# Optimization experiments

Hardware: AMD Instinct MI355X
Metric: run time of the kernel (lower is better)

Reference implementation:

```python
import jax, jax.numpy as jnp
from jax import lax
import numpy as np

B, Cin, Cout, H, W, K = 8, 128, 128, 64, 64, 3
K2 = K * K
STRIDE, PAD, DIL = 1, 1, 1
EPS = 1e-5


def setup_inputs() -> dict:
    key = jax.random.key(0)
    ks = jax.random.split(key, 9)
    fan_off = Cin * K2
    fan_def = Cin * K2
    x = jax.random.normal(ks[0], (B, Cin, H, W), jnp.float32)
    # small offset weights -> offsets of O(1) pixel, like early training
    offset_w = jax.random.normal(ks[1], (2 * K2, Cin, K, K), jnp.float32) / np.sqrt(fan_off)
    offset_b = 0.01 * jax.random.normal(ks[2], (2 * K2,), jnp.float32)
    deform_w = jax.random.normal(ks[3], (Cout, Cin, K, K), jnp.float32) / np.sqrt(fan_def)
    deform_b = 0.01 * jax.random.normal(ks[4], (Cout,), jnp.float32)
    gamma = 1.0 + 0.1 * jax.random.normal(ks[5], (Cout,), jnp.float32)
    beta = 0.1 * jax.random.normal(ks[6], (Cout,), jnp.float32)
    running_mean = 0.1 * jax.random.normal(ks[7], (Cout,), jnp.float32)
    running_var = jax.random.uniform(ks[8], (Cout,), jnp.float32, 0.5, 1.5)
    return {"x": x, "offset_w": offset_w, "offset_b": offset_b,
            "deform_w": deform_w, "deform_b": deform_b,
            "gamma": gamma, "beta": beta,
            "running_mean": running_mean, "running_var": running_var}


def _deform_block(x, offset_w, offset_b, deform_w, deform_b, gamma, beta, mean, var):
    # 1) offset prediction: standard 3x3 conv -> [B, 2*K2, Ho, Wo]
    offset = lax.conv_general_dilated(
        x, offset_w, window_strides=(STRIDE, STRIDE),
        padding=((PAD, PAD), (PAD, PAD)), rhs_dilation=(DIL, DIL),
        dimension_numbers=("NCHW", "OIHW", "NCHW"))
    offset = offset + offset_b[None, :, None, None]
    Ho, Wo = offset.shape[2], offset.shape[3]

    # torchvision layout: channel 2k -> dy, 2k+1 -> dx for kernel tap k
    off = offset.reshape(B, K2, 2, Ho, Wo)
    dy, dx = off[:, :, 0], off[:, :, 1]              # [B, K2, Ho, Wo]

    ky = (jnp.arange(K2) // K).astype(jnp.float32)
    kx = (jnp.arange(K2) % K).astype(jnp.float32)
    base_y = (jnp.arange(Ho, dtype=jnp.float32) * STRIDE - PAD)[None, :] + (ky * DIL)[:, None]  # [K2, Ho]
    base_x = (jnp.arange(Wo, dtype=jnp.float32) * STRIDE - PAD)[None, :] + (kx * DIL)[:, None]  # [K2, Wo]
    py = base_y[None, :, :, None] + dy               # [B, K2, Ho, Wo]
    px = base_x[None, :, None, :] + dx

    # 2) bilinear sampling with zero padding outside the image
    y0 = jnp.floor(py)
    x0 = jnp.floor(px)
    wy1 = py - y0; wy0 = 1.0 - wy1
    wx1 = px - x0; wx0 = 1.0 - wx1
    y0i = y0.astype(jnp.int32)
    x0i = x0.astype(jnp.int32)
    xf = x.reshape(B, Cin, H * W)

    def corner(yi, xi, wgt):
        valid = (yi >= 0) & (yi < H) & (xi >= 0) & (xi < W)
        idx = (jnp.clip(yi, 0, H - 1) * W + jnp.clip(xi, 0, W - 1)).reshape(B, 1, -1)
        g = jnp.take_along_axis(xf, idx, axis=2).reshape(B, Cin, K2, Ho, Wo)
        return g * (wgt * valid)[:, None]

    samp = (corner(y0i, x0i, wy0 * wx0)
            + corner(y0i, x0i + 1, wy0 * wx1)
            + corner(y0i + 1, x0i, wy1 * wx0)
            + corner(y0i + 1, x0i + 1, wy1 * wx1))   # [B, Cin, K2, Ho, Wo]

    # 3) conv-like accumulation over (Cin, K2)
    out = jnp.einsum("bckhw,ock->bohw", samp, deform_w.reshape(Cout, Cin, K2))
    out = out + deform_b[None, :, None, None]

    # 4) BatchNorm (inference, running stats) + SiLU
    scale = gamma / jnp.sqrt(var + EPS)
    out = (out - mean[None, :, None, None]) * scale[None, :, None, None] + beta[None, :, None, None]
    return out * jax.nn.sigmoid(out)


def reference(x, offset_w, offset_b, deform_w, deform_b, gamma, beta, running_mean, running_var):
    return _deform_block(x, offset_w, offset_b, deform_w, deform_b,
                         gamma, beta, running_mean, running_var)
```

## Files before the change

### kernel.cpp

```cpp
#include <hip/hip_runtime.h>

typedef float f32x4 __attribute__((ext_vector_type(4)));
typedef __bf16 bf16x8 __attribute__((ext_vector_type(8)));
typedef unsigned short u16x8 __attribute__((ext_vector_type(8)));

static constexpr int B_ = 8, Cin = 128, Cout = 128, K2 = 9;
static constexpr int HW  = 64 * 64;
static constexpr int CHW = Cin * HW;
static constexpr int KC  = Cin * K2;
static constexpr int SLD = 136;

static __device__ __forceinline__ unsigned short f2bf(float f) {
  unsigned int u = __builtin_bit_cast(unsigned int, f);
  u = u + 0x7fffu + ((u >> 16) & 1u);
  return (unsigned short)(u >> 16);
}
static __device__ __forceinline__ float b2f_lo(unsigned int u) {
  return __builtin_bit_cast(float, u << 16);
}
static __device__ __forceinline__ float b2f_hi(unsigned int u) {
  return __builtin_bit_cast(float, u & 0xffff0000u);
}
static __device__ __forceinline__ unsigned cvt_pk_bf16(float lo, float hi) {
  unsigned r;
  asm("v_cvt_pk_bf16_f32 %0, %1, %2" : "=v"(r) : "v"(lo), "v"(hi));
  return r;
}

__global__ __launch_bounds__(256) void prep_trans_kernel(
    const float* __restrict__ x, const float* __restrict__ dw,
    const float* __restrict__ ow, unsigned short* __restrict__ wsW2,
    unsigned short* __restrict__ wOffB2, unsigned short* __restrict__ xt) {
  int bid = blockIdx.x;
  int t = threadIdx.x;

  int swz = (bid & 7) * 64 + (bid >> 3);
  int b = swz >> 6, y = swz & 63;
  int lane = t & 63, cq = t >> 6;
  __shared__ unsigned short L[64 * SLD];
  const float* xb = x + b * CHW + y * 64;
#pragma unroll
  for (int i = 0; i < 32; ++i) {
    int c = i * 4 + cq;
    L[lane * SLD + c] = f2bf(xb[c * HW + lane]);
  }
  __syncthreads();
  int p = t >> 2, q = t & 3;
  unsigned short* op = xt + (size_t)b * HW * 128 + y * 64 * 128 + p * 128 + q * 32;
#pragma unroll
  for (int s = 0; s < 4; ++s)
    *(u16x8*)(op + s * 8) = *(const u16x8*)&L[p * SLD + q * 32 + s * 8];

  for (int i = bid * 256 + t; i < 8 * 9 * 4 * 512; i += 512 * 256) {
    int j = i & 7, ln = (i >> 3) & 63, ks = (i >> 9) & 3, t2 = i >> 11;
    int k = t2 % 9, w = t2 / 9;
    int oc = w * 16 + (ln & 15);
    int c = ks * 32 + (ln >> 4) * 8 + j;
    wsW2[i] = f2bf(dw[(oc * Cin + c) * K2 + k]);
  }
  {
    int i = bid * 256 + t;
    if (i < 9 * 4 * 2 * 512) {
      int j = i & 7, ln = (i >> 3) & 63, m = (i >> 9) & 1, t3 = i >> 10;
      int ks = t3 & 3, r = t3 >> 2;
      int oc = m * 16 + (ln & 15);
      int c = ks * 32 + (ln >> 4) * 8 + j;
      wOffB2[i] = (oc < 18) ? f2bf(ow[(oc * Cin + c) * K2 + r]) : (unsigned short)0;
    }
  }
}

__global__ __launch_bounds__(512, 4) void fused_kernel(
    const unsigned short* __restrict__ xt, const unsigned short* __restrict__ wsW2,
    const unsigned short* __restrict__ wOffB2, const float* __restrict__ ob,
    const float* __restrict__ dbias, const float* __restrict__ gamma,
    const float* __restrict__ beta, const float* __restrict__ mean,
    const float* __restrict__ var, float* __restrict__ out) {
  int bid = blockIdx.x;
  int swz = (bid & 7) * 64 + (bid >> 3);
  int b = swz >> 6, ho = swz & 63;
  int t = threadIdx.x;
  int lane = t & 63, wv = t >> 6;
  int col = lane & 15, g = lane >> 4;

  __shared__ unsigned short SAB[2][64 * SLD];
  __shared__ float T[64 * 20];
  __shared__ float RW4[576 * 4];
  __shared__ unsigned RI[576];

  const unsigned short* xtb = xt + (size_t)b * HW * 128;
  const unsigned int* xtb32 = (const unsigned int*)xtb;

  auto stageA = [&](int r, int buf) {
    int ky = r / 3, kx = r % 3;
    int yv = ho + ky - 1;
    bool oky = (unsigned)yv < 64u;
    int yc = min(max(yv, 0), 63);
#pragma unroll
    for (int rr = 0; rr < 8; ++rr) {
      int p = wv * 8 + rr;
      int xc = p + kx - 1;
      bool ok = oky && ((unsigned)xc < 64u);
      int xcc = min(max(xc, 0), 63);
      unsigned v = ok ? xtb32[(yc * 64 + xcc) * 64 + lane] : 0u;
      *(unsigned*)&SAB[buf][p * SLD + 2 * lane] = v;
    }
  };

  f32x4 accO = (f32x4){0.f, 0.f, 0.f, 0.f};
  int mA = wv >> 2, nA = wv & 3;

  stageA(0, 0);
  __syncthreads();
  for (int r = 0; r < 9; ++r) {
    int cur = r & 1;
    if (r < 8) stageA(r + 1, cur ^ 1);
#pragma unroll
    for (int ks = 0; ks < 4; ++ks) {
      bf16x8 bfr = *(const bf16x8*)&SAB[cur][(nA * 16 + col) * SLD + ks * 32 + g * 8];
      u16x8 af = *(const u16x8*)(wOffB2 + ((r * 4 + ks) * 2 + mA) * 512 + lane * 8);
      accO = __builtin_amdgcn_mfma_f32_16x16x32_bf16(
          __builtin_bit_cast(bf16x8, af), bfr, accO, 0, 0, 0);
    }
    __syncthreads();
  }
  {
#pragma unroll
    for (int rg = 0; rg < 4; ++rg) {
      int row = mA * 16 + g * 4 + rg;
      if (row < 18) T[(nA * 16 + col) * 20 + row] = accO[rg] + ob[row];
    }
  }
  __syncthreads();

#pragma unroll
  for (int it = 0; it < 2; ++it) {
    int idx = it * 64 + lane;
    if (idx < 72) {
      int k = idx >> 3, rr = idx & 7;
      int pp = wv * 8 + rr;
      float dy = T[pp * 20 + 2 * k], dx = T[pp * 20 + 2 * k + 1];
      float py = (float)(ho - 1 + k / 3) + dy;
      float px = (float)(pp - 1 + k % 3) + dx;
      float y0f = floorf(py), x0f = floorf(px);
      float wy1 = py - y0f, wy0 = 1.f - wy1;
      float wx1 = px - x0f, wx0 = 1.f - wx1;
      int y0 = (int)y0f, x0 = (int)x0f;
      bool vy0 = (unsigned)y0 < 64u, vy1 = (unsigned)(y0 + 1) < 64u;
      bool vx0 = (unsigned)x0 < 64u, vx1 = (unsigned)(x0 + 1) < 64u;
      float w00 = (vy0 && vx0) ? wy0 * wx0 : 0.f;
      float w01 = (vy0 && vx1) ? wy0 * wx1 : 0.f;
      float w10 = (vy1 && vx0) ? wy1 * wx0 : 0.f;
      float w11 = (vy1 && vx1) ? wy1 * wx1 : 0.f;
      int y0c = min(max(y0, 0), 63), y1c = min(max(y0 + 1, 0), 63);
      int xb2 = min(max(x0, 0), 62);
      unsigned pkw = (unsigned)(y0c * 64 + xb2) | ((unsigned)(y1c * 64 + xb2) << 12);
      if (x0 == 63) pkw |= (1u << 24);
      if (x0 == -1) pkw |= (1u << 25);
      int ridx = k * 64 + pp;
      RW4[ridx * 4 + 0] = w00; RW4[ridx * 4 + 1] = w01;
      RW4[ridx * 4 + 2] = w10; RW4[ridx * 4 + 3] = w11;
      RI[ridx] = pkw;
    }
  }
  __syncthreads();

  f32x4 acc[4];
#pragma unroll
  for (int j = 0; j < 4; ++j) acc[j] = (f32x4){0.f, 0.f, 0.f, 0.f};
  const unsigned short* wA = wsW2 + wv * (9 * 4 * 512) + lane * 8;

  {
#pragma unroll
    for (int r = 0; r < 8; ++r) {
      int pp = wv * 8 + r, ridx = pp;
      unsigned pk = RI[ridx];
      int o0 = pk & 4095, o1 = (pk >> 12) & 4095;
      bool s0 = (pk >> 24) & 1, s1 = (pk >> 25) & 1;
      const unsigned int* r0 = xtb32 + o0 * 64;
      const unsigned int* r1 = xtb32 + o1 * 64;
      unsigned c00 = r0[lane], c01 = r0[lane + 64];
      unsigned c10 = r1[lane], c11 = r1[lane + 64];
      unsigned a0 = s0 ? c01 : c00, a1 = s1 ? c00 : c01;
      unsigned a2 = s0 ? c11 : c10, a3 = s1 ? c10 : c11;
      float4 wv4 = *(const float4*)&RW4[ridx * 4];
      float lo = wv4.x * b2f_lo(a0) + wv4.y * b2f_lo(a1) + wv4.z * b2f_lo(a2) + wv4.w * b2f_lo(a3);
      float hi = wv4.x * b2f_hi(a0) + wv4.y * b2f_hi(a1) + wv4.z * b2f_hi(a2) + wv4.w * b2f_hi(a3);
      *(unsigned*)&SAB[0][pp * SLD + 2 * lane] = cvt_pk_bf16(lo, hi);
    }
  }
  __syncthreads();

  for (int k = 0; k < 9; ++k) {
    int cur = k & 1;
    unsigned c00[8], c01[8], c10[8], c11[8];
    if (k < 8) {
#pragma unroll
      for (int r = 0; r < 8; ++r) {
        int ridx = (k + 1) * 64 + wv * 8 + r;
        unsigned pk = RI[ridx];
        int o0 = pk & 4095, o1 = (pk >> 12) & 4095;
        const unsigned int* r0 = xtb32 + o0 * 64;
        const unsigned int* r1 = xtb32 + o1 * 64;
        c00[r] = r0[lane]; c01[r] = r0[lane + 64];
        c10[r] = r1[lane]; c11[r] = r1[lane + 64];
      }
    }
    u16x8 af[4];
#pragma unroll
    for (int ks = 0; ks < 4; ++ks)
      af[ks] = *(const u16x8*)(wA + (k * 4 + ks) * 512);
#pragma unroll
    for (int pt = 0; pt < 4; ++pt)
#pragma unroll
      for (int ks = 0; ks < 4; ++ks) {
        bf16x8 bfr = *(const bf16x8*)&SAB[cur][(pt * 16 + col) * SLD + ks * 32 + g * 8];
        acc[pt] = __builtin_amdgcn_mfma_f32_16x16x32_bf16(
            __builtin_bit_cast(bf16x8, af[ks]), bfr, acc[pt], 0, 0, 0);
      }
    if (k < 8) {
#pragma unroll
      for (int r = 0; r < 8; ++r) {
        int ridx = (k + 1) * 64 + wv * 8 + r;
        unsigned pk = RI[ridx];
        bool s0 = (pk >> 24) & 1, s1 = (pk >> 25) & 1;
        float4 wv4 = *(const float4*)&RW4[ridx * 4];
        unsigned a0 = s0 ? c01[r] : c00[r], a1 = s1 ? c00[r] : c01[r];
        unsigned a2 = s0 ? c11[r] : c10[r], a3 = s1 ? c10[r] : c11[r];
        float lo = wv4.x * b2f_lo(a0) + wv4.y * b2f_lo(a1) + wv4.z * b2f_lo(a2) + wv4.w * b2f_lo(a3);
        float hi = wv4.x * b2f_hi(a0) + wv4.y * b2f_hi(a1) + wv4.z * b2f_hi(a2) + wv4.w * b2f_hi(a3);
        *(unsigned*)&SAB[cur ^ 1][(wv * 8 + r) * SLD + 2 * lane] = cvt_pk_bf16(lo, hi);
      }
    }
    __syncthreads();
  }

  float* op = out + b * (Cout * HW) + ho * 64;
  int ocb = wv * 16 + g * 4;
#pragma unroll
  for (int r = 0; r < 4; ++r) {
    int oc = ocb + r;
    float sc = gamma[oc] * rsqrtf(var[oc] + 1e-5f);
    float bs = beta[oc] - mean[oc] * sc;
    float db = dbias[oc];
#pragma unroll
    for (int pt = 0; pt < 4; ++pt) {
      float v = (acc[pt][r] + db) * sc + bs;
      op[oc * HW + pt * 16 + col] = v / (1.f + __expf(-v));
    }
  }
}

extern "C" void kernel_launch(void* const* d_in, const int* in_sizes, int n_in,
                              void* d_out, int out_size, void* d_ws, size_t ws_size,
                              hipStream_t stream) {
  const float* x     = (const float*)d_in[0];
  const float* ow    = (const float*)d_in[1];
  const float* ob    = (const float*)d_in[2];
  const float* dw    = (const float*)d_in[3];
  const float* db    = (const float*)d_in[4];
  const float* gamma = (const float*)d_in[5];
  const float* beta  = (const float*)d_in[6];
  const float* mean  = (const float*)d_in[7];
  const float* var   = (const float*)d_in[8];

  char* wsc = (char*)d_ws;
  unsigned short* wsW2   = (unsigned short*)wsc;
  unsigned short* wOffB2 = (unsigned short*)(wsc + 294912);
  unsigned short* xt     = (unsigned short*)(wsc + 368640);

  prep_trans_kernel<<<512, 256, 0, stream>>>(x, dw, ow, wsW2, wOffB2, xt);
  fused_kernel<<<512, 512, 0, stream>>>(xt, wsW2, wOffB2, ob, db, gamma, beta,
                                        mean, var, (float*)d_out);
}
```

Measured before the change: 51.50 us.

## Pad transposed input to drop edge selects, prefetch weights, raise MFMA priority

Adds zero guard rows around the transposed bf16 input and stores biased offsets, so the bilinear gather no longer needs the per-corner edge-select logic. The next tap's weight fragments are now loaded one iteration ahead, overlapping with the current tap's MFMAs. The MFMA sections are wrapped in s_setprio so matrix work gets issue priority over the gather. This adds register pressure and relies on the padding layout staying in bounds, and it moves the workspace offset.

```diff
diff --git a/kernel.cpp b/kernel.cpp
--- a/kernel.cpp
+++ b/kernel.cpp
@@ -50,6 +50,11 @@
 #pragma unroll
   for (int s = 0; s < 4; ++s)
     *(u16x8*)(op + s * 8) = *(const u16x8*)&L[p * SLD + q * 32 + s * 8];
+
+  if (bid == 0 && t < 128) {
+    xt[-128 + t] = 0;
+    xt[(size_t)8 * HW * 128 + t] = 0;
+  }
 
   for (int i = bid * 256 + t; i < 8 * 9 * 4 * 512; i += 512 * 256) {
     int j = i & 7, ln = (i >> 3) & 63, ks = (i >> 9) & 3, t2 = i >> 11;
@@ -115,6 +120,7 @@
   for (int r = 0; r < 9; ++r) {
     int cur = r & 1;
     if (r < 8) stageA(r + 1, cur ^ 1);
+    __builtin_amdgcn_s_setprio(1);
 #pragma unroll
     for (int ks = 0; ks < 4; ++ks) {
       bf16x8 bfr = *(const bf16x8*)&SAB[cur][(nA * 16 + col) * SLD + ks * 32 + g * 8];
@@ -122,6 +128,7 @@
       accO = __builtin_amdgcn_mfma_f32_16x16x32_bf16(
           __builtin_bit_cast(bf16x8, af), bfr, accO, 0, 0, 0);
     }
+    __builtin_amdgcn_s_setprio(0);
     __syncthreads();
   }
   {
@@ -153,14 +160,13 @@
       float w10 = (vy1 && vx0) ? wy1 * wx0 : 0.f;
       float w11 = (vy1 && vx1) ? wy1 * wx1 : 0.f;
       int y0c = min(max(y0, 0), 63), y1c = min(max(y0 + 1, 0), 63);
-      int xb2 = min(max(x0, 0), 62);
-      unsigned pkw = (unsigned)(y0c * 64 + xb2) | ((unsigned)(y1c * 64 + xb2) << 12);
-      if (x0 == 63) pkw |= (1u << 24);
-      if (x0 == -1) pkw |= (1u << 25);
+      int x0c = min(max(x0, -1), 63);
+      unsigned o0p = (unsigned)(y0c * 64 + x0c + 1);
+      unsigned o1p = (unsigned)(y1c * 64 + x0c + 1);
       int ridx = k * 64 + pp;
+      RI[ridx] = o0p | (o1p << 13);
       RW4[ridx * 4 + 0] = w00; RW4[ridx * 4 + 1] = w01;
       RW4[ridx * 4 + 2] = w10; RW4[ridx * 4 + 3] = w11;
-      RI[ridx] = pkw;
     }
   }
   __syncthreads();
@@ -169,24 +175,33 @@
 #pragma unroll
   for (int j = 0; j < 4; ++j) acc[j] = (f32x4){0.f, 0.f, 0.f, 0.f};
   const unsigned short* wA = wsW2 + wv * (9 * 4 * 512) + lane * 8;
+
+  auto combineRec = [&](int ridx, unsigned c00, unsigned c01,
+                        unsigned c10, unsigned c11) -> unsigned {
+    float4 w4 = *(const float4*)&RW4[ridx * 4];
+    float lo = w4.x * b2f_lo(c00) + w4.y * b2f_lo(c01) +
+               w4.z * b2f_lo(c10) + w4.w * b2f_lo(c11);
+    float hi = w4.x * b2f_hi(c00) + w4.y * b2f_hi(c01) +
+               w4.z * b2f_hi(c10) + w4.w * b2f_hi(c11);
+    return cvt_pk_bf16(lo, hi);
+  };
+
+  u16x8 afc[4], afn[4];
+#pragma unroll
+  for (int ks = 0; ks < 4; ++ks)
+    afc[ks] = *(const u16x8*)(wA + ks * 512);
 
   {
 #pragma unroll
     for (int r = 0; r < 8; ++r) {
       int pp = wv * 8 + r, ridx = pp;
       unsigned pk = RI[ridx];
-      int o0 = pk & 4095, o1 = (pk >> 12) & 4095;
-      bool s0 = (pk >> 24) & 1, s1 = (pk >> 25) & 1;
+      int o0 = (int)(pk & 8191) - 1, o1 = (int)((pk >> 13) & 8191) - 1;
       const unsigned int* r0 = xtb32 + o0 * 64;
       const unsigned int* r1 = xtb32 + o1 * 64;
       unsigned c00 = r0[lane], c01 = r0[lane + 64];
       unsigned c10 = r1[lane], c11 = r1[lane + 64];
-      unsigned a0 = s0 ? c01 : c00, a1 = s1 ? c00 : c01;
-      unsigned a2 = s0 ? c11 : c10, a3 = s1 ? c10 : c11;
-      float4 wv4 = *(const float4*)&RW4[ridx * 4];
-      float lo = wv4.x * b2f_lo(a0) + wv4.y * b2f_lo(a1) + wv4.z * b2f_lo(a2) + wv4.w * b2f_lo(a3);
-      float hi = wv4.x * b2f_hi(a0) + wv4.y * b2f_hi(a1) + wv4.z * b2f_hi(a2) + wv4.w * b2f_hi(a3);
-      *(unsigned*)&SAB[0][pp * SLD + 2 * lane] = cvt_pk_bf16(lo, hi);
+      *(unsigned*)&SAB[0][pp * SLD + 2 * lane] = combineRec(ridx, c00, c01, c10, c11);
     }
   }
   __syncthreads();
@@ -199,38 +214,35 @@
       for (int r = 0; r < 8; ++r) {
         int ridx = (k + 1) * 64 + wv * 8 + r;
         unsigned pk = RI[ridx];
-        int o0 = pk & 4095, o1 = (pk >> 12) & 4095;
+        int o0 = (int)(pk & 8191) - 1, o1 = (int)((pk >> 13) & 8191) - 1;
         const unsigned int* r0 = xtb32 + o0 * 64;
         const unsigned int* r1 = xtb32 + o1 * 64;
         c00[r] = r0[lane]; c01[r] = r0[lane + 64];
         c10[r] = r1[lane]; c11[r] = r1[lane + 64];
       }
-    }
-    u16x8 af[4];
-#pragma unroll
-    for (int ks = 0; ks < 4; ++ks)
-      af[ks] = *(const u16x8*)(wA + (k * 4 + ks) * 512);
+#pragma unroll
+      for (int ks = 0; ks < 4; ++ks)
+        afn[ks] = *(const u16x8*)(wA + ((k + 1) * 4 + ks) * 512);
+    }
+    __builtin_amdgcn_s_setprio(1);
 #pragma unroll
     for (int pt = 0; pt < 4; ++pt)
 #pragma unroll
       for (int ks = 0; ks < 4; ++ks) {
         bf16x8 bfr = *(const bf16x8*)&SAB[cur][(pt * 16 + col) * SLD + ks * 32 + g * 8];
         acc[pt] = __builtin_amdgcn_mfma_f32_16x16x32_bf16(
-            __builtin_bit_cast(bf16x8, af[ks]), bfr, acc[pt], 0, 0, 0);
+            __builtin_bit_cast(bf16x8, afc[ks]), bfr, acc[pt], 0, 0, 0);
       }
+    __builtin_amdgcn_s_setprio(0);
     if (k < 8) {
 #pragma unroll
       for (int r = 0; r < 8; ++r) {
         int ridx = (k + 1) * 64 + wv * 8 + r;
-        unsigned pk = RI[ridx];
-        bool s0 = (pk >> 24) & 1, s1 = (pk >> 25) & 1;
-        float4 wv4 = *(const float4*)&RW4[ridx * 4];
-        unsigned a0 = s0 ? c01[r] : c00[r], a1 = s1 ? c00[r] : c01[r];
-        unsigned a2 = s0 ? c11[r] : c10[r], a3 = s1 ? c10[r] : c11[r];
-        float lo = wv4.x * b2f_lo(a0) + wv4.y * b2f_lo(a1) + wv4.z * b2f_lo(a2) + wv4.w * b2f_lo(a3);
-        float hi = wv4.x * b2f_hi(a0) + wv4.y * b2f_hi(a1) + wv4.z * b2f_hi(a2) + wv4.w * b2f_hi(a3);
-        *(unsigned*)&SAB[cur ^ 1][(wv * 8 + r) * SLD + 2 * lane] = cvt_pk_bf16(lo, hi);
+        *(unsigned*)&SAB[cur ^ 1][(wv * 8 + r) * SLD + 2 * lane] =
+            combineRec(ridx, c00[r], c01[r], c10[r], c11[r]);
       }
+#pragma unroll
+      for (int ks = 0; ks < 4; ++ks) afc[ks] = afn[ks];
     }
     __syncthreads();
   }
@@ -267,7 +279,7 @@
   char* wsc = (char*)d_ws;
   unsigned short* wsW2   = (unsigned short*)wsc;
   unsigned short* wOffB2 = (unsigned short*)(wsc + 294912);
-  unsigned short* xt     = (unsigned short*)(wsc + 368640);
+  unsigned short* xt     = (unsigned short*)(wsc + 368896);
 
   prep_trans_kernel<<<512, 256, 0, stream>>>(x, dw, ow, wsW2, wOffB2, xt);
   fused_kernel<<<512, 512, 0, stream>>>(xt, wsW2, wOffB2, ob, db, gamma, beta,
```

New measurement: 51.34 us. No clear change (-0.3%).
